# Kernel optimization log

Hardware: AMD Instinct MI355X
Metric: run time of the kernel (lower is better)

Reference implementation:

```python
import jax, jax.numpy as jnp
import numpy as np

# Structure matrix S (n_hos*n_types=6, n_structures=8) and internal int_S (unused in forward)
S_MAT = np.array([[1,0,1,0,0,1,0,1],[0,1,0,1,1,0,0,0],[1,1,0,0,0,0,1,0],[0,0,1,1,0,1,0,0],[0,1,1,0,1,0,0,1],[1,0,0,0,1,0,1,0]], dtype=np.float32)
CONTROL_STRENGTH = 10.0  # self.control_strength
PDHG_ITERS = 150         # fixed-iteration batched primal-dual LP solver
BATCH = 32768
N_STRUCT = 8
N_COMBO = 6


def setup_inputs() -> dict:
    key = jax.random.key(0)
    ks = jax.random.split(key, 9)
    X = jax.random.uniform(ks[0], (BATCH, 2, 3), jnp.float32)  # nonnegative bids
    def lin(k, fan_in, fan_out):
        return jax.random.normal(k, (fan_in, fan_out), jnp.float32) * (1.0 / np.sqrt(fan_in))
    W1 = lin(ks[1], 6, 20);  b1 = jnp.zeros((20,), jnp.float32)
    W2 = lin(ks[2], 20, 20); b2 = jnp.zeros((20,), jnp.float32)
    W3 = lin(ks[3], 20, 20); b3 = jnp.zeros((20,), jnp.float32)
    W4 = lin(ks[4], 20, 8);  b4 = jnp.zeros((8,), jnp.float32)
    S = jnp.asarray(S_MAT)
    return {"X": X, "W1": W1, "b1": b1, "W2": W2, "b2": b2, "W3": W3, "b3": b3,
            "W4": W4, "b4": b4, "S": S, "batch_size": BATCH}


def _mlp(Z, W1, b1, W2, b2, W3, b3, W4, b4):
    h = jnp.tanh(Z @ W1 + b1)
    h = jnp.tanh(h @ W2 + b2)
    h = jnp.tanh(h @ W3 + b3)
    return h @ W4 + b4  # [B, 8]


def _batched_lp(S, z, bvec):
    """Solve, per batch row: max 1'x - c*||x - z||_2  s.t. x>=0, S x <= b.
    Equivalent polytope A x <= b' with A=[S; -I], b'=[b; 0]; solved with PDHG.
    z, bvec: [B, 8], [B, 6]."""
    B = z.shape[0]
    A = jnp.concatenate([S, -jnp.eye(N_STRUCT, dtype=S.dtype)], axis=0)  # [14, 8]
    bfull = jnp.concatenate([bvec, jnp.zeros((B, N_STRUCT), bvec.dtype)], axis=1)  # [B, 14]
    L = jnp.linalg.norm(A)  # Frobenius norm upper-bounds spectral norm
    tau = 1.0 / L
    sigma = 1.0 / L

    def prox_g(v):
        # prox of g(x) = -1'x + c||x - z||_2 (w = ones): shift by tau*w then shrink toward z
        u = v + tau
        d = u - z
        n = jnp.linalg.norm(d, axis=-1, keepdims=True)
        scale = jnp.maximum(0.0, 1.0 - tau * CONTROL_STRENGTH / jnp.maximum(n, 1e-12))
        return z + scale * d

    x0 = jnp.maximum(z, 0.0)
    y0 = jnp.zeros((B, N_COMBO + N_STRUCT), z.dtype)

    def step(carry, _):
        x, xbar, y = carry
        y = jnp.maximum(0.0, y + sigma * (xbar @ A.T - bfull))  # dual ascent + proj >= 0
        x_new = prox_g(x - tau * (y @ A))                        # primal prox step
        return (x_new, 2.0 * x_new - x, y), None

    (x, _, _), _ = jax.lax.scan(step, (x0, x0, y0), None, length=PDHG_ITERS)
    return x


def reference(X, W1, b1, W2, b2, W3, b3, W4, b4, S, batch_size):
    B = X.shape[0]
    Z = X.reshape(B, N_COMBO)              # view(-1, n_hos*n_types)
    z = _mlp(Z, W1, b1, W2, b2, W3, b3, W4, b4)  # neural_net_forward -> [B, 8]
    x1 = _batched_lp(S, z, Z)              # linear_program_forward (W = ones)
    return x1
```

## Files before the change

### kernel.cpp

```cpp
#include <hip/hip_runtime.h>
#include <math.h>


#define N_ITERS 150

__device__ __forceinline__ float fast_tanh(float a) {
    float e = __expf(2.0f * a);
    return 1.0f - 2.0f * __builtin_amdgcn_rcpf(e + 1.0f);
}

__device__ __forceinline__ float dpp_swap(float v) {
    union { float f; int i; } u;
    u.f = v;
    u.i = __builtin_amdgcn_update_dpp(0, u.i, 0xB1, 0xF, 0xF, true);
    return u.f;
}

__global__ void __launch_bounds__(64)
__attribute__((amdgpu_waves_per_eu(1, 1)))
matchnet_kernel(
    const float* __restrict__ X,
    const float* __restrict__ W1, const float* __restrict__ b1,
    const float* __restrict__ W2, const float* __restrict__ b2,
    const float* __restrict__ W3, const float* __restrict__ b3,
    const float* __restrict__ W4, const float* __restrict__ b4,
    float* __restrict__ out, int B)
{
    __shared__ float sW1[120], sW2[400], sW3[400], sW4[160];
    __shared__ float sb1[20], sb2[20], sb3[20], sb4[8];
    for (int i = threadIdx.x; i < 120; i += blockDim.x) sW1[i] = W1[i];
    for (int i = threadIdx.x; i < 400; i += blockDim.x) sW2[i] = W2[i];
    for (int i = threadIdx.x; i < 400; i += blockDim.x) sW3[i] = W3[i];
    for (int i = threadIdx.x; i < 160; i += blockDim.x) sW4[i] = W4[i];
    if (threadIdx.x < 20) {
        sb1[threadIdx.x] = b1[threadIdx.x];
        sb2[threadIdx.x] = b2[threadIdx.x];
        sb3[threadIdx.x] = b3[threadIdx.x];
    }
    if (threadIdx.x < 8) sb4[threadIdx.x] = b4[threadIdx.x];
    __syncthreads();

    int gidx = blockIdx.x * blockDim.x + threadIdx.x;
    int row = gidx >> 1;
    if (row >= B) return;
    const bool isOdd = (gidx & 1) != 0;

    float bb0 = X[row * 6 + 0], bb1 = X[row * 6 + 1], bb2 = X[row * 6 + 2];
    float bb3 = X[row * 6 + 3], bb4 = X[row * 6 + 4], bb5 = X[row * 6 + 5];

    float h1[20], h2[20];
    #pragma unroll
    for (int j = 0; j < 20; j++) {
        float acc = sb1[j];
        acc = fmaf(bb0, sW1[0 * 20 + j], acc);
        acc = fmaf(bb1, sW1[1 * 20 + j], acc);
        acc = fmaf(bb2, sW1[2 * 20 + j], acc);
        acc = fmaf(bb3, sW1[3 * 20 + j], acc);
        acc = fmaf(bb4, sW1[4 * 20 + j], acc);
        acc = fmaf(bb5, sW1[5 * 20 + j], acc);
        h1[j] = fast_tanh(acc);
    }
    #pragma unroll
    for (int j = 0; j < 20; j++) {
        float acc = sb2[j];
        #pragma unroll
        for (int i = 0; i < 20; i++) acc = fmaf(h1[i], sW2[i * 20 + j], acc);
        h2[j] = fast_tanh(acc);
    }
    #pragma unroll
    for (int j = 0; j < 20; j++) {
        float acc = sb3[j];
        #pragma unroll
        for (int i = 0; i < 20; i++) acc = fmaf(h2[i], sW3[i * 20 + j], acc);
        h1[j] = fast_tanh(acc);
    }
    float z[8];
    #pragma unroll
    for (int k = 0; k < 8; k++) {
        float acc = sb4[k];
        #pragma unroll
        for (int i = 0; i < 20; i++) acc = fmaf(h1[i], sW4[i * 8 + k], acc);
        z[k] = acc;
    }

    const float tau  = 0.18898223650461363f;
    const float c    = 0.03571428571428571f;
    const float tauC = 1.8898223650461363f;

    float oz0 = isOdd ? z[4] : z[0];
    float oz1 = isOdd ? z[5] : z[1];
    float oz2 = isOdd ? z[6] : z[2];
    float oz3 = isOdd ? z[7] : z[3];

    float ot0 = tau - oz0, ot1 = tau - oz1, ot2 = tau - oz2, ot3 = tau - oz3;
    float oTI0 = ot0, oTI1 = ot1, oTI2 = ot2, oTI3 = ot3;

    float ox0 = fmaxf(oz0, 0.f), ox1 = fmaxf(oz1, 0.f);
    float ox2 = fmaxf(oz2, 0.f), ox3 = fmaxf(oz3, 0.f);
    float oxb0 = ox0, oxb1 = ox1, oxb2 = ox2, oxb3 = ox3;

    float cb0 = c * bb0, cb1 = c * bb1, cb2 = c * bb2;
    float cb3 = c * bb3, cb4 = c * bb4, cb5 = c * bb5;
    float cbq0 = isOdd ? cb4 : cb0;
    float cbq1 = isOdd ? cb3 : cb2;
    float cbq2 = isOdd ? cb5 : cb1;
    float Yq0 = 0.f, Yq1 = 0.f, Yq2 = 0.f;

    #pragma unroll 1
    for (int it = 0; it < N_ITERS; it++) {
        float rxb0 = dpp_swap(oxb0), rxb1 = dpp_swap(oxb1);
        float rxb2 = dpp_swap(oxb2), rxb3 = dpp_swap(oxb3);

        float op_a = oxb0 + rxb1;
        float op_b = oxb2 + rxb3;
        float op_c = oxb3 + rxb2;
        float op_d = isOdd ? op_c : op_b;
        float sq0  = op_a + op_d;
        float op_e = oxb1 + rxb2;
        float op_f = isOdd ? rxb3 : oxb0;
        float sq1  = op_e + op_f;
        float op_g = oxb1 + oxb3;
        float op_h = oxb0 + oxb2;
        float op_i = isOdd ? op_h : op_g;
        float sq2  = op_i + rxb0;

        Yq0 = fmaxf(0.f, fmaf(c, sq0, Yq0) - cbq0);
        Yq1 = fmaxf(0.f, fmaf(c, sq1, Yq1) - cbq1);
        Yq2 = fmaxf(0.f, fmaf(c, sq2, Yq2) - cbq2);

        float rY0 = dpp_swap(Yq0), rY1 = dpp_swap(Yq1), rY2 = dpp_swap(Yq2);

        float op_j = Yq0 + rY2;
        float op_k = isOdd ? Yq2 : Yq1;
        float colq0 = op_j + op_k;
        float op_l = Yq1 + rY0;
        float op_p = isOdd ? 0.f : Yq2;
        float colq1 = op_l + op_p;
        float op_m = Yq0 + rY0;
        float op_n = rY1 + Yq2;
        float op_o = op_m + rY1;
        float colq2 = isOdd ? op_n : op_o;
        float colq3 = isOdd ? op_m : op_n;

        oTI0 = fmaxf(ot0, fmaf(-c, oxb0, oTI0));
        oTI1 = fmaxf(ot1, fmaf(-c, oxb1, oTI1));
        oTI2 = fmaxf(ot2, fmaf(-c, oxb2, oTI2));
        oTI3 = fmaxf(ot3, fmaf(-c, oxb3, oTI3));

        float od0 = (ox0 + oTI0) - colq0;
        float od1 = (ox1 + oTI1) - colq1;
        float od2 = (ox2 + oTI2) - colq2;
        float od3 = (ox3 + oTI3) - colq3;

        float nl = od0 * od0;
        nl = fmaf(od1, od1, nl);
        nl = fmaf(od2, od2, nl);
        nl = fmaf(od3, od3, nl);
        float rn = dpp_swap(nl);
        float nsq = nl + rn;

        float rs = __builtin_amdgcn_rsqf(nsq);
        float scale = fmaxf(0.f, fmaf(-tauC, rs, 1.f));

        float xn0 = fmaf(scale, od0, oz0);
        float xn1 = fmaf(scale, od1, oz1);
        float xn2 = fmaf(scale, od2, oz2);
        float xn3 = fmaf(scale, od3, oz3);
        oxb0 = fmaf(2.f, xn0, -ox0); ox0 = xn0;
        oxb1 = fmaf(2.f, xn1, -ox1); ox1 = xn1;
        oxb2 = fmaf(2.f, xn2, -ox2); ox2 = xn2;
        oxb3 = fmaf(2.f, xn3, -ox3); ox3 = xn3;
    }

    float4* out4 = (float4*)out;
    out4[gidx] = make_float4(ox0, ox1, ox2, ox3);
}

extern "C" void kernel_launch(void* const* d_in, const int* in_sizes, int n_in,
                              void* d_out, int out_size, void* d_ws, size_t ws_size,
                              hipStream_t stream) {
    const float* X  = (const float*)d_in[0];
    const float* W1 = (const float*)d_in[1];
    const float* b1 = (const float*)d_in[2];
    const float* W2 = (const float*)d_in[3];
    const float* b2 = (const float*)d_in[4];
    const float* W3 = (const float*)d_in[5];
    const float* b3 = (const float*)d_in[6];
    const float* W4 = (const float*)d_in[7];
    const float* b4 = (const float*)d_in[8];
    float* out = (float*)d_out;

    int B = in_sizes[0] / 6;
    const int block = 64;
    long long threads = (long long)B * 2;
    int grid = (int)((threads + block - 1) / block);
    hipLaunchKernelGGL(matchnet_kernel, dim3(grid), dim3(block), 0, stream,
                       X, W1, b1, W2, b2, W3, b3, W4, b4, out, B);
}
```

Baseline: 104.6 us.

## Split MLP neurons across paired lanes with transposed vectorized LDS weights

Before, both lanes of each row pair computed the full 20-wide MLP redundantly. Now each lane computes half the neurons of every layer, and the halves are swapped between the pair with DPP. The weights are stored transposed in LDS so each neuron's weights can be read with 128-bit vector loads. This halves the per-thread MLP FLOPs and LDS reads, at the cost of per-lane dynamic LDS offsets, DPP exchanges and selects after each layer.

Result: faster. 102.4 us (median of 2 runs) (-2.1%).

```diff
diff --git a/kernel.cpp b/kernel.cpp
--- a/kernel.cpp
+++ b/kernel.cpp
@@ -3,6 +3,8 @@
 
 
 #define N_ITERS 150
+typedef float f2 __attribute__((ext_vector_type(2)));
+typedef float f4 __attribute__((ext_vector_type(4)));
 
 __device__ __forceinline__ float fast_tanh(float a) {
     float e = __expf(2.0f * a);
@@ -26,71 +28,113 @@
     const float* __restrict__ W4, const float* __restrict__ b4,
     float* __restrict__ out, int B)
 {
-    __shared__ float sW1[120], sW2[400], sW3[400], sW4[160];
-    __shared__ float sb1[20], sb2[20], sb3[20], sb4[8];
-    for (int i = threadIdx.x; i < 120; i += blockDim.x) sW1[i] = W1[i];
-    for (int i = threadIdx.x; i < 400; i += blockDim.x) sW2[i] = W2[i];
-    for (int i = threadIdx.x; i < 400; i += blockDim.x) sW3[i] = W3[i];
-    for (int i = threadIdx.x; i < 160; i += blockDim.x) sW4[i] = W4[i];
-    if (threadIdx.x < 20) {
-        sb1[threadIdx.x] = b1[threadIdx.x];
-        sb2[threadIdx.x] = b2[threadIdx.x];
-        sb3[threadIdx.x] = b3[threadIdx.x];
-    }
-    if (threadIdx.x < 8) sb4[threadIdx.x] = b4[threadIdx.x];
+    __shared__ alignas(16) float tW1[160], tW2[400], tW3[400], tW4[160];
+    __shared__ alignas(16) float sb1[20], sb2[20], sb3[20], sb4[8];
+    {
+        int tid = threadIdx.x;
+        for (int idx = tid; idx < 120; idx += 64) { int i = idx / 20, j = idx % 20; tW1[j * 8 + i] = W1[idx]; }
+        for (int idx = tid; idx < 400; idx += 64) { int i = idx / 20, j = idx % 20; tW2[j * 20 + i] = W2[idx]; }
+        for (int idx = tid; idx < 400; idx += 64) { int i = idx / 20, j = idx % 20; tW3[j * 20 + i] = W3[idx]; }
+        for (int idx = tid; idx < 160; idx += 64) { int i = idx / 8,  k = idx % 8;  tW4[k * 20 + i] = W4[idx]; }
+        if (tid < 20) { sb1[tid] = b1[tid]; sb2[tid] = b2[tid]; sb3[tid] = b3[tid]; }
+        if (tid < 8) sb4[tid] = b4[tid];
+    }
     __syncthreads();
 
     int gidx = blockIdx.x * blockDim.x + threadIdx.x;
     int row = gidx >> 1;
     if (row >= B) return;
     const bool isOdd = (gidx & 1) != 0;
+    const int jb = isOdd ? 10 : 0;
+    const int kb = isOdd ? 4 : 0;
 
     float bb0 = X[row * 6 + 0], bb1 = X[row * 6 + 1], bb2 = X[row * 6 + 2];
     float bb3 = X[row * 6 + 3], bb4 = X[row * 6 + 4], bb5 = X[row * 6 + 5];
 
-    float h1[20], h2[20];
+    float hA[10], hB[10];
+    {
+        float acc[10];
+        const f2* bv = (const f2*)&sb1[jb];
+        #pragma unroll
+        for (int p = 0; p < 5; p++) { f2 b = bv[p]; acc[2 * p] = b.x; acc[2 * p + 1] = b.y; }
+        #pragma unroll
+        for (int n = 0; n < 10; n++) {
+            int j = jb + n;
+            f4 w0 = *(const f4*)&tW1[j * 8];
+            f2 w1 = *(const f2*)&tW1[j * 8 + 4];
+            float a = acc[n];
+            a = fmaf(bb0, w0.x, a); a = fmaf(bb1, w0.y, a); a = fmaf(bb2, w0.z, a);
+            a = fmaf(bb3, w0.w, a); a = fmaf(bb4, w1.x, a); a = fmaf(bb5, w1.y, a);
+            acc[n] = fast_tanh(a);
+        }
+        #pragma unroll
+        for (int n = 0; n < 10; n++) {
+            float t = dpp_swap(acc[n]);
+            hA[n] = isOdd ? t : acc[n];
+            hB[n] = isOdd ? acc[n] : t;
+        }
+    }
     #pragma unroll
-    for (int j = 0; j < 20; j++) {
-        float acc = sb1[j];
-        acc = fmaf(bb0, sW1[0 * 20 + j], acc);
-        acc = fmaf(bb1, sW1[1 * 20 + j], acc);
-        acc = fmaf(bb2, sW1[2 * 20 + j], acc);
-        acc = fmaf(bb3, sW1[3 * 20 + j], acc);
-        acc = fmaf(bb4, sW1[4 * 20 + j], acc);
-        acc = fmaf(bb5, sW1[5 * 20 + j], acc);
-        h1[j] = fast_tanh(acc);
-    }
-    #pragma unroll
-    for (int j = 0; j < 20; j++) {
-        float acc = sb2[j];
-        #pragma unroll
-        for (int i = 0; i < 20; i++) acc = fmaf(h1[i], sW2[i * 20 + j], acc);
-        h2[j] = fast_tanh(acc);
-    }
-    #pragma unroll
-    for (int j = 0; j < 20; j++) {
-        float acc = sb3[j];
-        #pragma unroll
-        for (int i = 0; i < 20; i++) acc = fmaf(h2[i], sW3[i * 20 + j], acc);
-        h1[j] = fast_tanh(acc);
-    }
-    float z[8];
-    #pragma unroll
-    for (int k = 0; k < 8; k++) {
-        float acc = sb4[k];
-        #pragma unroll
-        for (int i = 0; i < 20; i++) acc = fmaf(h1[i], sW4[i * 8 + k], acc);
-        z[k] = acc;
+    for (int layer = 0; layer < 2; layer++) {
+        const float* tw = layer ? tW3 : tW2;
+        const float* sb = layer ? sb3 : sb2;
+        float acc[10];
+        const f2* bv = (const f2*)&sb[jb];
+        #pragma unroll
+        for (int p = 0; p < 5; p++) { f2 b = bv[p]; acc[2 * p] = b.x; acc[2 * p + 1] = b.y; }
+        #pragma unroll
+        for (int n = 0; n < 10; n++) {
+            int j = jb + n;
+            const f4* w = (const f4*)&tw[j * 20];
+            f4 w0 = w[0], w1 = w[1], w2 = w[2], w3 = w[3], w4 = w[4];
+            float a = acc[n];
+            a = fmaf(hA[0], w0.x, a); a = fmaf(hA[1], w0.y, a);
+            a = fmaf(hA[2], w0.z, a); a = fmaf(hA[3], w0.w, a);
+            a = fmaf(hA[4], w1.x, a); a = fmaf(hA[5], w1.y, a);
+            a = fmaf(hA[6], w1.z, a); a = fmaf(hA[7], w1.w, a);
+            a = fmaf(hA[8], w2.x, a); a = fmaf(hA[9], w2.y, a);
+            a = fmaf(hB[0], w2.z, a); a = fmaf(hB[1], w2.w, a);
+            a = fmaf(hB[2], w3.x, a); a = fmaf(hB[3], w3.y, a);
+            a = fmaf(hB[4], w3.z, a); a = fmaf(hB[5], w3.w, a);
+            a = fmaf(hB[6], w4.x, a); a = fmaf(hB[7], w4.y, a);
+            a = fmaf(hB[8], w4.z, a); a = fmaf(hB[9], w4.w, a);
+            acc[n] = fast_tanh(a);
+        }
+        #pragma unroll
+        for (int n = 0; n < 10; n++) {
+            float t = dpp_swap(acc[n]);
+            hA[n] = isOdd ? t : acc[n];
+            hB[n] = isOdd ? acc[n] : t;
+        }
+    }
+    float oz0, oz1, oz2, oz3;
+    {
+        f4 b = *(const f4*)&sb4[kb];
+        float acc[4] = {b.x, b.y, b.z, b.w};
+        #pragma unroll
+        for (int n = 0; n < 4; n++) {
+            int k = kb + n;
+            const f4* w = (const f4*)&tW4[k * 20];
+            f4 w0 = w[0], w1 = w[1], w2 = w[2], w3 = w[3], w4 = w[4];
+            float a = acc[n];
+            a = fmaf(hA[0], w0.x, a); a = fmaf(hA[1], w0.y, a);
+            a = fmaf(hA[2], w0.z, a); a = fmaf(hA[3], w0.w, a);
+            a = fmaf(hA[4], w1.x, a); a = fmaf(hA[5], w1.y, a);
+            a = fmaf(hA[6], w1.z, a); a = fmaf(hA[7], w1.w, a);
+            a = fmaf(hA[8], w2.x, a); a = fmaf(hA[9], w2.y, a);
+            a = fmaf(hB[0], w2.z, a); a = fmaf(hB[1], w2.w, a);
+            a = fmaf(hB[2], w3.x, a); a = fmaf(hB[3], w3.y, a);
+            a = fmaf(hB[4], w3.z, a); a = fmaf(hB[5], w3.w, a);
+            a = fmaf(hB[6], w4.x, a); a = fmaf(hB[7], w4.y, a);
+            a = fmaf(hB[8], w4.z, a); a = fmaf(hB[9], w4.w, a);
+            acc[n] = a;
+        }
+        oz0 = acc[0]; oz1 = acc[1]; oz2 = acc[2]; oz3 = acc[3];
     }
 
     const float tau  = 0.18898223650461363f;
     const float c    = 0.03571428571428571f;
     const float tauC = 1.8898223650461363f;
-
-    float oz0 = isOdd ? z[4] : z[0];
-    float oz1 = isOdd ? z[5] : z[1];
-    float oz2 = isOdd ? z[6] : z[2];
-    float oz3 = isOdd ? z[7] : z[3];
 
     float ot0 = tau - oz0, ot1 = tau - oz1, ot2 = tau - oz2, ot3 = tau - oz3;
     float oTI0 = ot0, oTI1 = ot1, oTI2 = ot2, oTI3 = ot3;
```
